# Kernel tuning notes

Measured on AMD Instinct MI355X. Metric: run time of the kernel, lower is better.

The kernel has to match this reference:

```python
import jax, jax.numpy as jnp
import numpy as np

B, S, D, H = 4, 2048, 1024, 16
HD = D // H  # head dim = 64


def setup_inputs() -> dict:
    key = jax.random.key(0)
    ks = jax.random.split(key, 10)
    sd = 1.0 / np.sqrt(D)
    return {
        "x": jax.random.normal(ks[0], (B, S, D), jnp.float32),
        "Wq": jax.random.normal(ks[1], (D, D), jnp.float32) * sd,
        "Wk": jax.random.normal(ks[2], (D, D), jnp.float32) * sd,
        "Wv": jax.random.normal(ks[3], (D, D), jnp.float32) * sd,
        "in_w": jax.random.normal(ks[4], (3 * D, D), jnp.float32) * sd,
        "in_b": jax.random.normal(ks[5], (3 * D,), jnp.float32) * 0.01,
        "out_w": jax.random.normal(ks[6], (D, D), jnp.float32) * sd,
        "out_b": jax.random.normal(ks[7], (D,), jnp.float32) * 0.01,
        "proj_w": jax.random.normal(ks[8], (D, D), jnp.float32) * sd,
        "proj_b": jax.random.normal(ks[9], (D,), jnp.float32) * 0.01,
    }


def _attn_block(x, Wq, Wk, Wv, in_w, in_b, out_w, out_b, proj_w, proj_b):
    b, s, d = x.shape
    # redundant pre-projections (bias-free)
    q = jnp.einsum('bsd,ed->bse', x, Wq)
    k = jnp.einsum('bsd,ed->bse', x, Wk)
    v = jnp.einsum('bsd,ed->bse', x, Wv)
    # MultiheadAttention internal in-projection (with bias)
    wq, wk, wv = in_w[:d], in_w[d:2 * d], in_w[2 * d:]
    bq, bk, bv = in_b[:d], in_b[d:2 * d], in_b[2 * d:]
    Q = jnp.einsum('bse,fe->bsf', q, wq) + bq
    K = jnp.einsum('bse,fe->bsf', k, wk) + bk
    V = jnp.einsum('bse,fe->bsf', v, wv) + bv
    # split heads -> [b, h, s, hd]
    Q = Q.reshape(b, s, H, HD).transpose(0, 2, 1, 3)
    K = K.reshape(b, s, H, HD).transpose(0, 2, 1, 3)
    V = V.reshape(b, s, H, HD).transpose(0, 2, 1, 3)
    scale = 1.0 / np.sqrt(HD)
    scores = jnp.einsum('bhqd,bhkd->bhqk', Q * scale, K)
    # FAITHFUL quirk: float tril mask (ones / zeros) is ADDED to scores,
    # exactly as torch does with a float attn_mask (not a -inf causal mask).
    mask = jnp.tril(jnp.ones((s, s), scores.dtype))
    scores = scores + mask
    A = jax.nn.softmax(scores, axis=-1)
    ctx = jnp.einsum('bhqk,bhkd->bhqd', A, V)
    ctx = ctx.transpose(0, 2, 1, 3).reshape(b, s, d)
    attn = jnp.einsum('bse,fe->bsf', ctx, out_w) + out_b  # out_proj
    out = jnp.einsum('bse,fe->bsf', attn, proj_w) + proj_b  # self.project
    return x + out


def reference(x, Wq, Wk, Wv, in_w, in_b, out_w, out_b, proj_w, proj_b):
    return _attn_block(x, Wq, Wk, Wv, in_w, in_b, out_w, out_b, proj_w, proj_b)
```

## Files before the change

kernel.cpp:

```cpp
#include <hip/hip_runtime.h>
#include <stdint.h>

typedef unsigned short u16;
typedef __attribute__((ext_vector_type(8))) short bfx8;
typedef __attribute__((ext_vector_type(4))) float fx4;
typedef __attribute__((ext_vector_type(16))) float fx16;

static __device__ __forceinline__ u16 f2b(float f) {
  union { float f; uint32_t u; } v; v.f = f;
  uint32_t r = v.u + 0x7fffu + ((v.u >> 16) & 1u);
  return (u16)(r >> 16);
}

static __device__ __forceinline__ uint32_t cvtpk(float lo, float hi) {
  uint32_t r;
  asm("v_cvt_pk_bf16_f32 %0, %1, %2" : "=v"(r) : "v"(lo), "v"(hi));
  return r;
}

static __device__ __forceinline__ float ex2(float x) {
  float r;
  asm("v_exp_f32 %0, %1" : "=v"(r) : "v"(x));
  return r;
}

static __device__ __forceinline__ void gload16(const void* g, void* lds) {
  __builtin_amdgcn_global_load_lds((const __attribute__((address_space(1))) uint32_t*)g,
                                   (__attribute__((address_space(3))) uint32_t*)lds,
                                   16, 0, 0);
}

__global__ __launch_bounds__(256) void f32_to_bf16_k(const float* __restrict__ in,
                                                     u16* __restrict__ out, int n) {
  int i = (blockIdx.x * 256 + threadIdx.x) * 8;
  if (i >= n) return;
  float4 a = *(const float4*)(in + i);
  float4 b = *(const float4*)(in + i + 4);
  bfx8 o;
  o[0]=(short)f2b(a.x); o[1]=(short)f2b(a.y); o[2]=(short)f2b(a.z); o[3]=(short)f2b(a.w);
  o[4]=(short)f2b(b.x); o[5]=(short)f2b(b.y); o[6]=(short)f2b(b.z); o[7]=(short)f2b(b.w);
  *(bfx8*)(out + i) = o;
}

struct TransArgs { const float* in[4]; u16* out[4]; };
__global__ __launch_bounds__(256) void transpose4_k(TransArgs ta) {
  const float* in = ta.in[blockIdx.z];
  u16* out = ta.out[blockIdx.z];
  __shared__ u16 t[64][65];
  const int bx = blockIdx.x * 64, by = blockIdx.y * 64;
  const int tid = threadIdx.x;
#pragma unroll
  for (int i = 0; i < 16; ++i) {
    int idx = tid + i * 256; int r = idx >> 6, c = idx & 63;
    t[c][r] = f2b(in[(size_t)(by + r) * 1024 + bx + c]);
  }
  __syncthreads();
#pragma unroll
  for (int i = 0; i < 16; ++i) {
    int idx = tid + i * 256; int r = idx >> 6, c = idx & 63;
    out[(size_t)(bx + r) * 1024 + by + c] = t[r][c];
  }
}

__global__ __launch_bounds__(256) void make_b2_k(const float* __restrict__ pw,
                                                 const float* __restrict__ ob,
                                                 const float* __restrict__ pb,
                                                 float* __restrict__ b2) {
  const int f = blockIdx.x, tid = threadIdx.x;
  float s = 0.f;
  for (int e = tid; e < 1024; e += 256) s += pw[(size_t)f * 1024 + e] * ob[e];
#pragma unroll
  for (int d = 1; d < 64; d <<= 1) s += __shfl_xor(s, d);
  __shared__ float red[4];
  if ((tid & 63) == 0) red[tid >> 6] = s;
  __syncthreads();
  if (tid == 0) b2[f] = red[0] + red[1] + red[2] + red[3] + pb[f];
}

static __device__ __forceinline__ void gemm_core(const u16* __restrict__ A,
                                                 const u16* __restrict__ Bt,
                                                 int K, int bm, int bn,
                                                 u16* As, u16* Bs, fx4 (&acc)[4][4]) {
  const int tid = threadIdx.x, w = tid >> 6, l = tid & 63, lm = l & 15, lk = l >> 4;
  const int wm = w >> 1, wn = w & 1;
  const int nkt = K >> 6;
  for (int kt = 0; kt < nkt; ++kt) {
#pragma unroll
    for (int i = 0; i < 4; ++i) {
      int off = i * 4096 + w * 1024;
      int loff = off + l * 16;
      int row = loff >> 7, cb = loff & 127;
      gload16((const char*)A + ((size_t)(bm * 128 + row) * K + kt * 64) * 2 + cb,
              (char*)As + off);
      gload16((const char*)Bt + ((size_t)(bn * 128 + row) * K + kt * 64) * 2 + cb,
              (char*)Bs + off);
    }
    __syncthreads();
#pragma unroll
    for (int kk = 0; kk < 2; ++kk) {
      bfx8 a[4], b[4];
#pragma unroll
      for (int mi = 0; mi < 4; ++mi)
        a[mi] = *(const bfx8*)((const char*)As + (wm * 64 + mi * 16 + lm) * 128 + lk * 16 + kk * 64);
#pragma unroll
      for (int nj = 0; nj < 4; ++nj)
        b[nj] = *(const bfx8*)((const char*)Bs + (wn * 64 + nj * 16 + lm) * 128 + lk * 16 + kk * 64);
#pragma unroll
      for (int mi = 0; mi < 4; ++mi)
#pragma unroll
        for (int nj = 0; nj < 4; ++nj)
          acc[mi][nj] = __builtin_amdgcn_mfma_f32_16x16x32_bf16(a[mi], b[nj], acc[mi][nj], 0, 0, 0);
    }
    __syncthreads();
  }
}

struct CombArgs { const u16* A[4]; const u16* Bt[4]; u16* C[4]; };
__global__ __launch_bounds__(256) void gemm_combine_k(CombArgs ca) {
  const int z = blockIdx.z;
  __shared__ u16 As[8192], Bs[8192];
  fx4 acc[4][4];
#pragma unroll
  for (int mi = 0; mi < 4; ++mi)
#pragma unroll
    for (int nj = 0; nj < 4; ++nj) acc[mi][nj] = 0.f;
  gemm_core(ca.A[z], ca.Bt[z], 1024, blockIdx.x, blockIdx.y, As, Bs, acc);
  const int tid = threadIdx.x, w = tid >> 6, l = tid & 63, lm = l & 15, lk = l >> 4;
  const int wm = w >> 1, wn = w & 1;
  u16* C = ca.C[z];
#pragma unroll
  for (int mi = 0; mi < 4; ++mi)
#pragma unroll
    for (int nj = 0; nj < 4; ++nj)
#pragma unroll
      for (int r = 0; r < 4; ++r) {
        int m = blockIdx.x * 128 + wm * 64 + mi * 16 + lk * 4 + r;
        int n = blockIdx.y * 128 + wn * 64 + nj * 16 + lm;
        C[(size_t)m * 1024 + n] = f2b(acc[mi][nj][r]);
      }
}

__global__ __launch_bounds__(256) void gemm_qkv_k(const u16* __restrict__ xb,
                                                  const u16* __restrict__ Wc,
                                                  const float* __restrict__ bias,
                                                  u16* __restrict__ Qh, u16* __restrict__ Kh,
                                                  u16* __restrict__ Vh) {
  const int bl = blockIdx.x;
  const int xcd = bl & 7, local = bl >> 3;
  const int bm = xcd * 8 + (local & 7);
  const int bn = local >> 3;
  __shared__ u16 As[8192], Bs[8192];
  fx4 acc[4][4];
#pragma unroll
  for (int mi = 0; mi < 4; ++mi)
#pragma unroll
    for (int nj = 0; nj < 4; ++nj) acc[mi][nj] = 0.f;
  gemm_core(xb, Wc, 1024, bm, bn, As, Bs, acc);
  const int tid = threadIdx.x, w = tid >> 6, l = tid & 63, lm = l & 15, lk = l >> 4;
  const int wm = w >> 1, wn = w & 1;
  const int t = bn >> 3;
  u16* dst = (t == 0) ? Qh : ((t == 1) ? Kh : Vh);
#pragma unroll
  for (int mi = 0; mi < 4; ++mi)
#pragma unroll
    for (int nj = 0; nj < 4; ++nj)
#pragma unroll
      for (int r = 0; r < 4; ++r) {
        int m = bm * 128 + wm * 64 + mi * 16 + lk * 4 + r;
        int n = bn * 128 + wn * 64 + nj * 16 + lm;
        float v = acc[mi][nj][r] + bias[n];
        int f = n & 1023, h = f >> 6, hd = f & 63, b = m >> 11, s = m & 2047;
        size_t hb = ((size_t)(b * 16 + h)) * 131072;
        size_t idx;
        if (t == 2) {
          int sl = s & 63, st = s >> 6;
          idx = hb + (size_t)st * 4096 + (size_t)(hd * 64 + (sl ^ ((hd & 7) << 3)));
        } else if (t == 1) {
          idx = hb + (size_t)s * 64 + (hd ^ ((s & 7) << 3));
        } else {
          idx = hb + (size_t)s * 64 + hd;
        }
        dst[idx] = f2b(v);
      }
}

__global__ __launch_bounds__(256) void gemm_final_k(const u16* __restrict__ ctx,
                                                    const u16* __restrict__ W2,
                                                    const float* __restrict__ b2,
                                                    const float* __restrict__ x,
                                                    float* __restrict__ out) {
  const int bl = blockIdx.x;
  const int xcd = bl & 7, local = bl >> 3;
  const int bm = xcd * 8 + (local & 7);
  const int bn = local >> 3;
  __shared__ u16 As[8192], Bs[8192];
  fx4 acc[4][4];
#pragma unroll
  for (int mi = 0; mi < 4; ++mi)
#pragma unroll
    for (int nj = 0; nj < 4; ++nj) acc[mi][nj] = 0.f;
  gemm_core(ctx, W2, 1024, bm, bn, As, Bs, acc);
  const int tid = threadIdx.x, w = tid >> 6, l = tid & 63, lm = l & 15, lk = l >> 4;
  const int wm = w >> 1, wn = w & 1;
#pragma unroll
  for (int mi = 0; mi < 4; ++mi)
#pragma unroll
    for (int nj = 0; nj < 4; ++nj)
#pragma unroll
      for (int r = 0; r < 4; ++r) {
        int m = bm * 128 + wm * 64 + mi * 16 + lk * 4 + r;
        int n = bn * 128 + wn * 64 + nj * 16 + lm;
        size_t idx = (size_t)m * 1024 + n;
        out[idx] = acc[mi][nj][r] + b2[n] + x[idx];
      }
}

__global__ __launch_bounds__(512, 4) void attn_k(const u16* __restrict__ Qh,
                                                 const u16* __restrict__ Kh,
                                                 const u16* __restrict__ Vh,
                                                 u16* __restrict__ ctx) {
  const int bl = blockIdx.x;
  const int wk = (bl & 7) * 64 + (bl >> 3);
  const int bh = wk >> 3, qt = wk & 7;
  const int tid = threadIdx.x, w = tid >> 6, l = tid & 63;
  const int ql = l & 31, h = l >> 5;
  __shared__ __align__(16) u16 Ks[2][4096];
  __shared__ __align__(16) u16 Vs[2][4096];

  const float SC = 0.18033688011112042f;
  const float MA = 1.4426950408889634f;
  const float THR = 11.541560327111708f;

  const size_t base = (size_t)bh * 131072;
  const int qb = qt * 256 + w * 32;
  const int q = qb + ql;
  bfx8 qf[4];
  {
    const u16* qp = Qh + base + (size_t)q * 64 + 8 * h;
    qf[0] = *(const bfx8*)(qp);
    qf[1] = *(const bfx8*)(qp + 16);
    qf[2] = *(const bfx8*)(qp + 32);
    qf[3] = *(const bfx8*)(qp + 48);
  }
  float m_run = -1024.f, l_part = 0.f;
  fx16 accO[2];
  accO[0] = 0.f; accO[1] = 0.f;

  const char* Kg = (const char*)(Kh + base);
  const char* Vg = (const char*)(Vh + base);
  const int o = tid * 16;
  const int sw8 = (ql & 7) << 4;

#define STAGE(t, s)                                            \
  {                                                            \
    gload16(Kg + (size_t)(t) * 8192 + o, (char*)Ks[s] + o);    \
    gload16(Vg + (size_t)(t) * 8192 + o, (char*)Vs[s] + o);    \
  }

  STAGE(0, 0);
  asm volatile("s_waitcnt vmcnt(0)" ::: "memory");
  __builtin_amdgcn_s_barrier();
  __builtin_amdgcn_sched_barrier(0);

  int cur = 0;
  for (int kt = 0; kt < 32; ++kt) {
    if (kt + 1 < 32) STAGE(kt + 1, cur ^ 1);
    __builtin_amdgcn_sched_barrier(0);

    const char* Kc = (const char*)Ks[cur];
    const char* Vc = (const char*)Vs[cur];

    fx16 sS[2];
    sS[0] = 0.f; sS[1] = 0.f;
    __builtin_amdgcn_s_setprio(1);
#pragma unroll
    for (int ks = 0; ks < 4; ++ks) {
      bfx8 kf0 = *(const bfx8*)(Kc + (0 * 32 + ql) * 128 + (((ks << 5) | (h << 4)) ^ sw8));
      bfx8 kf1 = *(const bfx8*)(Kc + (1 * 32 + ql) * 128 + (((ks << 5) | (h << 4)) ^ sw8));
      sS[0] = __builtin_amdgcn_mfma_f32_32x32x16_bf16(kf0, qf[ks], sS[0], 0, 0, 0);
      sS[1] = __builtin_amdgcn_mfma_f32_32x32x16_bf16(kf1, qf[ks], sS[1], 0, 0, 0);
    }
    __builtin_amdgcn_s_setprio(0);

    const int dk = kt - (qb >> 6);
    {
      float cO = -m_run, cI = cO + MA;
      if (dk < 0) {
#pragma unroll
        for (int r = 0; r < 16; ++r) {
          sS[0][r] = fmaf(sS[0][r], SC, cI);
          sS[1][r] = fmaf(sS[1][r], SC, cI);
        }
      } else if (dk > 0) {
#pragma unroll
        for (int r = 0; r < 16; ++r) {
          sS[0][r] = fmaf(sS[0][r], SC, cO);
          sS[1][r] = fmaf(sS[1][r], SC, cO);
        }
      } else {
#pragma unroll
        for (int kb = 0; kb < 2; ++kb)
#pragma unroll
          for (int r = 0; r < 16; ++r) {
            int key = kt * 64 + kb * 32 + (r & 3) + 8 * (r >> 2) + 4 * h;
            sS[kb][r] = fmaf(sS[kb][r], SC, (key <= q) ? cI : cO);
          }
      }
    }
    float mx;
    {
      float m0 = fmaxf(fmaxf(sS[0][0], sS[0][1]), fmaxf(sS[0][2], sS[0][3]));
      float m1 = fmaxf(fmaxf(sS[0][4], sS[0][5]), fmaxf(sS[0][6], sS[0][7]));
      float m2 = fmaxf(fmaxf(sS[0][8], sS[0][9]), fmaxf(sS[0][10], sS[0][11]));
      float m3 = fmaxf(fmaxf(sS[0][12], sS[0][13]), fmaxf(sS[0][14], sS[0][15]));
      float m4 = fmaxf(fmaxf(sS[1][0], sS[1][1]), fmaxf(sS[1][2], sS[1][3]));
      float m5 = fmaxf(fmaxf(sS[1][4], sS[1][5]), fmaxf(sS[1][6], sS[1][7]));
      float m6 = fmaxf(fmaxf(sS[1][8], sS[1][9]), fmaxf(sS[1][10], sS[1][11]));
      float m7 = fmaxf(fmaxf(sS[1][12], sS[1][13]), fmaxf(sS[1][14], sS[1][15]));
      mx = fmaxf(fmaxf(fmaxf(m0, m1), fmaxf(m2, m3)), fmaxf(fmaxf(m4, m5), fmaxf(m6, m7)));
    }
    float full = fmaxf(mx, __shfl_xor(mx, 32));
    if (!__all(full <= THR)) {
      float d = fmaxf(full, 0.f);
      float corr = ex2(-d);
      m_run += d;
      l_part *= corr;
#pragma unroll
      for (int r = 0; r < 16; ++r) {
        int rq = (r & 3) + 8 * (r >> 2) + 4 * h;
        float cr = __shfl(corr, (l & 32) | rq);
        accO[0][r] *= cr;
        accO[1][r] *= cr;
        sS[0][r] -= d;
        sS[1][r] -= d;
      }
    }
    fx16 tt;
#pragma unroll
    for (int r = 0; r < 16; ++r) {
      sS[0][r] = ex2(sS[0][r]);
      sS[1][r] = ex2(sS[1][r]);
      tt[r] = sS[0][r] + sS[1][r];
    }
    {
      float ls0 = tt[0] + tt[8],  ls1 = tt[1] + tt[9];
      float ls2 = tt[2] + tt[10], ls3 = tt[3] + tt[11];
      float ls4 = tt[4] + tt[12], ls5 = tt[5] + tt[13];
      float ls6 = tt[6] + tt[14], ls7 = tt[7] + tt[15];
      l_part += ((ls0 + ls4) + (ls1 + ls5)) + ((ls2 + ls6) + (ls3 + ls7));
    }
    uint32_t pw[8][2];
#pragma unroll
    for (int kb = 0; kb < 2; ++kb)
#pragma unroll
      for (int gg = 0; gg < 4; ++gg) {
        pw[kb * 4 + gg][0] = cvtpk(sS[kb][4 * gg + 0], sS[kb][4 * gg + 1]);
        pw[kb * 4 + gg][1] = cvtpk(sS[kb][4 * gg + 2], sS[kb][4 * gg + 3]);
      }

    __builtin_amdgcn_s_setprio(1);
#pragma unroll
    for (int ks = 0; ks < 4; ++ks) {
      union { uint32_t u[4]; bfx8 v; } pa;
#pragma unroll
      for (int p = 0; p < 2; ++p) {
        uint32_t contrib = h ? pw[2 * ks][p] : pw[2 * ks + 1][p];
        uint32_t rcv = __shfl_xor(contrib, 32);
        pa.u[p]     = h ? rcv : pw[2 * ks][p];
        pa.u[2 + p] = h ? pw[2 * ks + 1][p] : rcv;
      }
      bfx8 vf0 = *(const bfx8*)(Vc + (0 * 32 + ql) * 128 + (((ks << 5) | (h << 4)) ^ sw8));
      bfx8 vf1 = *(const bfx8*)(Vc + (1 * 32 + ql) * 128 + (((ks << 5) | (h << 4)) ^ sw8));
      accO[0] = __builtin_amdgcn_mfma_f32_32x32x16_bf16(pa.v, vf0, accO[0], 0, 0, 0);
      accO[1] = __builtin_amdgcn_mfma_f32_32x32x16_bf16(pa.v, vf1, accO[1], 0, 0, 0);
    }
    __builtin_amdgcn_s_setprio(0);

    asm volatile("s_waitcnt vmcnt(0)" ::: "memory");
    __builtin_amdgcn_s_barrier();
    __builtin_amdgcn_sched_barrier(0);
    cur ^= 1;
  }
#undef STAGE

  float inv = 1.0f / (l_part + __shfl_xor(l_part, 32));
  const int b = bh >> 4, hcol = bh & 15;
#pragma unroll
  for (int r = 0; r < 16; ++r) {
    int rq = (r & 3) + 8 * (r >> 2) + 4 * h;
    float invq = __shfl(inv, (l & 32) | rq);
    size_t rowb = ((size_t)b * 2048 + (qb + rq)) * 1024 + hcol * 64 + ql;
    ctx[rowb]      = f2b(accO[0][r] * invq);
    ctx[rowb + 32] = f2b(accO[1][r] * invq);
  }
}

extern "C" void kernel_launch(void* const* d_in, const int* in_sizes, int n_in,
                              void* d_out, int out_size, void* d_ws, size_t ws_size,
                              hipStream_t stream) {
  (void)in_sizes; (void)n_in; (void)out_size; (void)ws_size;
  const float* x      = (const float*)d_in[0];
  const float* Wq     = (const float*)d_in[1];
  const float* Wk     = (const float*)d_in[2];
  const float* Wv     = (const float*)d_in[3];
  const float* in_w   = (const float*)d_in[4];
  const float* in_b   = (const float*)d_in[5];
  const float* out_w  = (const float*)d_in[6];
  const float* out_b  = (const float*)d_in[7];
  const float* proj_w = (const float*)d_in[8];
  const float* proj_b = (const float*)d_in[9];
  float* out = (float*)d_out;

  char* ws = (char*)d_ws;
  const size_t MB = 1ull << 20;
  u16* xb   = (u16*)(ws);
  u16* ctx  = xb;
  u16* Qh   = (u16*)(ws + 16 * MB);
  u16* Kh   = (u16*)(ws + 32 * MB);
  u16* Vh   = (u16*)(ws + 48 * MB);
  u16* inwb = Kh;
  u16* tmpT = Vh;
  u16* pwb  = (u16*)(ws + 48 * MB + 8 * MB);
  u16* Wc   = (u16*)(ws + 64 * MB);
  u16* W2   = (u16*)(ws + 70 * MB);
  float* b2 = (float*)(ws + 72 * MB);

  f32_to_bf16_k<<<4096, 256, 0, stream>>>(x, xb, 8388608);
  f32_to_bf16_k<<<1536, 256, 0, stream>>>(in_w, inwb, 3145728);
  f32_to_bf16_k<<<512, 256, 0, stream>>>(proj_w, pwb, 1048576);

  TransArgs ta;
  ta.in[0] = Wq; ta.in[1] = Wk; ta.in[2] = Wv; ta.in[3] = out_w;
  for (int z = 0; z < 4; ++z) ta.out[z] = tmpT + (size_t)z * 1048576;
  transpose4_k<<<dim3(16, 16, 4), 256, 0, stream>>>(ta);

  CombArgs ca;
  ca.A[0] = inwb; ca.A[1] = inwb + 1048576; ca.A[2] = inwb + 2097152; ca.A[3] = pwb;
  for (int z = 0; z < 4; ++z) ca.Bt[z] = tmpT + (size_t)z * 1048576;
  ca.C[0] = Wc; ca.C[1] = Wc + 1048576; ca.C[2] = Wc + 2097152; ca.C[3] = W2;
  gemm_combine_k<<<dim3(8, 8, 4), 256, 0, stream>>>(ca);

  make_b2_k<<<1024, 256, 0, stream>>>(proj_w, out_b, proj_b, b2);

  gemm_qkv_k<<<1536, 256, 0, stream>>>(xb, Wc, in_b, Qh, Kh, Vh);
  attn_k<<<512, 512, 0, stream>>>(Qh, Kh, Vh, ctx);
  gemm_final_k<<<512, 256, 0, stream>>>(ctx, W2, b2, x, out);
}
```

Before: 266.2 us.

## Double attention K/V stage size, merge convert launches, bf16 residual read

The attention kernel now stages 128 keys per double-buffered step instead of 64 and processes them as two 64-key sub-tiles. This halves the number of wait-plus-barrier points per block, at the cost of doubling LDS per block, which may lower occupancy. The three fp32-to-bf16 conversion launches are merged into one kernel to cut launch overhead. When the workspace is large enough, ctx gets its own buffer and the final GEMM reads the residual from the bf16 copy of x instead of fp32 x. That halves residual traffic but adds bf16 rounding error to the output.

```diff
diff --git a/kernel.cpp b/kernel.cpp
--- a/kernel.cpp
+++ b/kernel.cpp
@@ -12,6 +12,11 @@
   return (u16)(r >> 16);
 }
 
+static __device__ __forceinline__ float b2f(u16 u) {
+  union { uint32_t u; float f; } v; v.u = ((uint32_t)u) << 16;
+  return v.f;
+}
+
 static __device__ __forceinline__ uint32_t cvtpk(float lo, float hi) {
   uint32_t r;
   asm("v_cvt_pk_bf16_f32 %0, %1, %2" : "=v"(r) : "v"(lo), "v"(hi));
@@ -30,16 +35,21 @@
                                    16, 0, 0);
 }
 
-__global__ __launch_bounds__(256) void f32_to_bf16_k(const float* __restrict__ in,
-                                                     u16* __restrict__ out, int n) {
-  int i = (blockIdx.x * 256 + threadIdx.x) * 8;
-  if (i >= n) return;
-  float4 a = *(const float4*)(in + i);
-  float4 b = *(const float4*)(in + i + 4);
+struct Cv3 { const float* in0; u16* out0; const float* in1; u16* out1;
+             const float* in2; u16* out2; };
+__global__ __launch_bounds__(256) void convert3_k(Cv3 a) {
+  const int b = blockIdx.x;
+  const float* in; u16* out; int i;
+  if (b < 4096)      { in = a.in0; out = a.out0; i = b; }
+  else if (b < 5632) { in = a.in1; out = a.out1; i = b - 4096; }
+  else               { in = a.in2; out = a.out2; i = b - 5632; }
+  int idx = (i * 256 + threadIdx.x) * 8;
+  float4 x = *(const float4*)(in + idx);
+  float4 y = *(const float4*)(in + idx + 4);
   bfx8 o;
-  o[0]=(short)f2b(a.x); o[1]=(short)f2b(a.y); o[2]=(short)f2b(a.z); o[3]=(short)f2b(a.w);
-  o[4]=(short)f2b(b.x); o[5]=(short)f2b(b.y); o[6]=(short)f2b(b.z); o[7]=(short)f2b(b.w);
-  *(bfx8*)(out + i) = o;
+  o[0]=(short)f2b(x.x); o[1]=(short)f2b(x.y); o[2]=(short)f2b(x.z); o[3]=(short)f2b(x.w);
+  o[4]=(short)f2b(y.x); o[5]=(short)f2b(y.y); o[6]=(short)f2b(y.z); o[7]=(short)f2b(y.w);
+  *(bfx8*)(out + idx) = o;
 }
 
 struct TransArgs { const float* in[4]; u16* out[4]; };
@@ -188,6 +198,7 @@
                                                     const u16* __restrict__ W2,
                                                     const float* __restrict__ b2,
                                                     const float* __restrict__ x,
+                                                    const u16* __restrict__ resid16,
                                                     float* __restrict__ out) {
   const int bl = blockIdx.x;
   const int xcd = bl & 7, local = bl >> 3;
@@ -211,7 +222,8 @@
         int m = bm * 128 + wm * 64 + mi * 16 + lk * 4 + r;
         int n = bn * 128 + wn * 64 + nj * 16 + lm;
         size_t idx = (size_t)m * 1024 + n;
-        out[idx] = acc[mi][nj][r] + b2[n] + x[idx];
+        float res = resid16 ? b2f(resid16[idx]) : x[idx];
+        out[idx] = acc[mi][nj][r] + b2[n] + res;
       }
 }
 
@@ -224,8 +236,8 @@
   const int bh = wk >> 3, qt = wk & 7;
   const int tid = threadIdx.x, w = tid >> 6, l = tid & 63;
   const int ql = l & 31, h = l >> 5;
-  __shared__ __align__(16) u16 Ks[2][4096];
-  __shared__ __align__(16) u16 Vs[2][4096];
+  __shared__ __align__(16) u16 Ks[2][8192];
+  __shared__ __align__(16) u16 Vs[2][8192];
 
   const float SC = 0.18033688011112042f;
   const float MA = 1.4426950408889634f;
@@ -251,10 +263,12 @@
   const int o = tid * 16;
   const int sw8 = (ql & 7) << 4;
 
-#define STAGE(t, s)                                            \
-  {                                                            \
-    gload16(Kg + (size_t)(t) * 8192 + o, (char*)Ks[s] + o);    \
-    gload16(Vg + (size_t)(t) * 8192 + o, (char*)Vs[s] + o);    \
+#define STAGE(t, s)                                                          \
+  {                                                                          \
+    gload16(Kg + (size_t)(t) * 16384 + o,        (char*)Ks[s] + o);          \
+    gload16(Kg + (size_t)(t) * 16384 + o + 8192, (char*)Ks[s] + o + 8192);   \
+    gload16(Vg + (size_t)(t) * 16384 + o,        (char*)Vs[s] + o);          \
+    gload16(Vg + (size_t)(t) * 16384 + o + 8192, (char*)Vs[s] + o + 8192);   \
   }
 
   STAGE(0, 0);
@@ -263,118 +277,122 @@
   __builtin_amdgcn_sched_barrier(0);
 
   int cur = 0;
-  for (int kt = 0; kt < 32; ++kt) {
-    if (kt + 1 < 32) STAGE(kt + 1, cur ^ 1);
+  for (int kt = 0; kt < 16; ++kt) {
+    if (kt + 1 < 16) STAGE(kt + 1, cur ^ 1);
     __builtin_amdgcn_sched_barrier(0);
 
-    const char* Kc = (const char*)Ks[cur];
-    const char* Vc = (const char*)Vs[cur];
-
-    fx16 sS[2];
-    sS[0] = 0.f; sS[1] = 0.f;
-    __builtin_amdgcn_s_setprio(1);
-#pragma unroll
-    for (int ks = 0; ks < 4; ++ks) {
-      bfx8 kf0 = *(const bfx8*)(Kc + (0 * 32 + ql) * 128 + (((ks << 5) | (h << 4)) ^ sw8));
-      bfx8 kf1 = *(const bfx8*)(Kc + (1 * 32 + ql) * 128 + (((ks << 5) | (h << 4)) ^ sw8));
-      sS[0] = __builtin_amdgcn_mfma_f32_32x32x16_bf16(kf0, qf[ks], sS[0], 0, 0, 0);
-      sS[1] = __builtin_amdgcn_mfma_f32_32x32x16_bf16(kf1, qf[ks], sS[1], 0, 0, 0);
+#pragma unroll
+    for (int sub = 0; sub < 2; ++sub) {
+      const char* Kc = (const char*)Ks[cur] + sub * 8192;
+      const char* Vc = (const char*)Vs[cur] + sub * 8192;
+      const int kt2 = kt * 2 + sub;
+
+      fx16 sS[2];
+      sS[0] = 0.f; sS[1] = 0.f;
+      __builtin_amdgcn_s_setprio(1);
+#pragma unroll
+      for (int ks = 0; ks < 4; ++ks) {
+        bfx8 kf0 = *(const bfx8*)(Kc + (0 * 32 + ql) * 128 + (((ks << 5) | (h << 4)) ^ sw8));
+        bfx8 kf1 = *(const bfx8*)(Kc + (1 * 32 + ql) * 128 + (((ks << 5) | (h << 4)) ^ sw8));
+        sS[0] = __builtin_amdgcn_mfma_f32_32x32x16_bf16(kf0, qf[ks], sS[0], 0, 0, 0);
+        sS[1] = __builtin_amdgcn_mfma_f32_32x32x16_bf16(kf1, qf[ks], sS[1], 0, 0, 0);
+      }
+      __builtin_amdgcn_s_setprio(0);
+
+      const int dk = kt2 - (qb >> 6);
+      {
+        float cO = -m_run, cI = cO + MA;
+        if (dk < 0) {
+#pragma unroll
+          for (int r = 0; r < 16; ++r) {
+            sS[0][r] = fmaf(sS[0][r], SC, cI);
+            sS[1][r] = fmaf(sS[1][r], SC, cI);
+          }
+        } else if (dk > 0) {
+#pragma unroll
+          for (int r = 0; r < 16; ++r) {
+            sS[0][r] = fmaf(sS[0][r], SC, cO);
+            sS[1][r] = fmaf(sS[1][r], SC, cO);
+          }
+        } else {
+#pragma unroll
+          for (int kb = 0; kb < 2; ++kb)
+#pragma unroll
+            for (int r = 0; r < 16; ++r) {
+              int key = kt2 * 64 + kb * 32 + (r & 3) + 8 * (r >> 2) + 4 * h;
+              sS[kb][r] = fmaf(sS[kb][r], SC, (key <= q) ? cI : cO);
+            }
+        }
+      }
+      float mx;
+      {
+        float m0 = fmaxf(fmaxf(sS[0][0], sS[0][1]), fmaxf(sS[0][2], sS[0][3]));
+        float m1 = fmaxf(fmaxf(sS[0][4], sS[0][5]), fmaxf(sS[0][6], sS[0][7]));
+        float m2 = fmaxf(fmaxf(sS[0][8], sS[0][9]), fmaxf(sS[0][10], sS[0][11]));
+        float m3 = fmaxf(fmaxf(sS[0][12], sS[0][13]), fmaxf(sS[0][14], sS[0][15]));
+        float m4 = fmaxf(fmaxf(sS[1][0], sS[1][1]), fmaxf(sS[1][2], sS[1][3]));
+        float m5 = fmaxf(fmaxf(sS[1][4], sS[1][5]), fmaxf(sS[1][6], sS[1][7]));
+        float m6 = fmaxf(fmaxf(sS[1][8], sS[1][9]), fmaxf(sS[1][10], sS[1][11]));
+        float m7 = fmaxf(fmaxf(sS[1][12], sS[1][13]), fmaxf(sS[1][14], sS[1][15]));
+        mx = fmaxf(fmaxf(fmaxf(m0, m1), fmaxf(m2, m3)), fmaxf(fmaxf(m4, m5), fmaxf(m6, m7)));
+      }
+      float full = fmaxf(mx, __shfl_xor(mx, 32));
+      if (!__all(full <= THR)) {
+        float d = fmaxf(full, 0.f);
+        float corr = ex2(-d);
+        m_run += d;
+        l_part *= corr;
+#pragma unroll
+        for (int r = 0; r < 16; ++r) {
+          int rq = (r & 3) + 8 * (r >> 2) + 4 * h;
+          float cr = __shfl(corr, (l & 32) | rq);
+          accO[0][r] *= cr;
+          accO[1][r] *= cr;
+          sS[0][r] -= d;
+          sS[1][r] -= d;
+        }
+      }
+      fx16 tt;
+#pragma unroll
+      for (int r = 0; r < 16; ++r) {
+        sS[0][r] = ex2(sS[0][r]);
+        sS[1][r] = ex2(sS[1][r]);
+        tt[r] = sS[0][r] + sS[1][r];
+      }
+      {
+        float ls0 = tt[0] + tt[8],  ls1 = tt[1] + tt[9];
+        float ls2 = tt[2] + tt[10], ls3 = tt[3] + tt[11];
+        float ls4 = tt[4] + tt[12], ls5 = tt[5] + tt[13];
+        float ls6 = tt[6] + tt[14], ls7 = tt[7] + tt[15];
+        l_part += ((ls0 + ls4) + (ls1 + ls5)) + ((ls2 + ls6) + (ls3 + ls7));
+      }
+      uint32_t pw[8][2];
+#pragma unroll
+      for (int kb = 0; kb < 2; ++kb)
+#pragma unroll
+        for (int gg = 0; gg < 4; ++gg) {
+          pw[kb * 4 + gg][0] = cvtpk(sS[kb][4 * gg + 0], sS[kb][4 * gg + 1]);
+          pw[kb * 4 + gg][1] = cvtpk(sS[kb][4 * gg + 2], sS[kb][4 * gg + 3]);
+        }
+
+      __builtin_amdgcn_s_setprio(1);
+#pragma unroll
+      for (int ks = 0; ks < 4; ++ks) {
+        union { uint32_t u[4]; bfx8 v; } pa;
+#pragma unroll
+        for (int p = 0; p < 2; ++p) {
+          uint32_t contrib = h ? pw[2 * ks][p] : pw[2 * ks + 1][p];
+          uint32_t rcv = __shfl_xor(contrib, 32);
+          pa.u[p]     = h ? rcv : pw[2 * ks][p];
+          pa.u[2 + p] = h ? pw[2 * ks + 1][p] : rcv;
+        }
+        bfx8 vf0 = *(const bfx8*)(Vc + (0 * 32 + ql) * 128 + (((ks << 5) | (h << 4)) ^ sw8));
+        bfx8 vf1 = *(const bfx8*)(Vc + (1 * 32 + ql) * 128 + (((ks << 5) | (h << 4)) ^ sw8));
+        accO[0] = __builtin_amdgcn_mfma_f32_32x32x16_bf16(pa.v, vf0, accO[0], 0, 0, 0);
+        accO[1] = __builtin_amdgcn_mfma_f32_32x32x16_bf16(pa.v, vf1, accO[1], 0, 0, 0);
+      }
+      __builtin_amdgcn_s_setprio(0);
     }
-    __builtin_amdgcn_s_setprio(0);
-
-    const int dk = kt - (qb >> 6);
-    {
-      float cO = -m_run, cI = cO + MA;
-      if (dk < 0) {
-#pragma unroll
-        for (int r = 0; r < 16; ++r) {
-          sS[0][r] = fmaf(sS[0][r], SC, cI);
-          sS[1][r] = fmaf(sS[1][r], SC, cI);
-        }
-      } else if (dk > 0) {
-#pragma unroll
-        for (int r = 0; r < 16; ++r) {
-          sS[0][r] = fmaf(sS[0][r], SC, cO);
-          sS[1][r] = fmaf(sS[1][r], SC, cO);
-        }
-      } else {
-#pragma unroll
-        for (int kb = 0; kb < 2; ++kb)
-#pragma unroll
-          for (int r = 0; r < 16; ++r) {
-            int key = kt * 64 + kb * 32 + (r & 3) + 8 * (r >> 2) + 4 * h;
-            sS[kb][r] = fmaf(sS[kb][r], SC, (key <= q) ? cI : cO);
-          }
-      }
-    }
-    float mx;
-    {
-      float m0 = fmaxf(fmaxf(sS[0][0], sS[0][1]), fmaxf(sS[0][2], sS[0][3]));
-      float m1 = fmaxf(fmaxf(sS[0][4], sS[0][5]), fmaxf(sS[0][6], sS[0][7]));
-      float m2 = fmaxf(fmaxf(sS[0][8], sS[0][9]), fmaxf(sS[0][10], sS[0][11]));
-      float m3 = fmaxf(fmaxf(sS[0][12], sS[0][13]), fmaxf(sS[0][14], sS[0][15]));
-      float m4 = fmaxf(fmaxf(sS[1][0], sS[1][1]), fmaxf(sS[1][2], sS[1][3]));
-      float m5 = fmaxf(fmaxf(sS[1][4], sS[1][5]), fmaxf(sS[1][6], sS[1][7]));
-      float m6 = fmaxf(fmaxf(sS[1][8], sS[1][9]), fmaxf(sS[1][10], sS[1][11]));
-      float m7 = fmaxf(fmaxf(sS[1][12], sS[1][13]), fmaxf(sS[1][14], sS[1][15]));
-      mx = fmaxf(fmaxf(fmaxf(m0, m1), fmaxf(m2, m3)), fmaxf(fmaxf(m4, m5), fmaxf(m6, m7)));
-    }
-    float full = fmaxf(mx, __shfl_xor(mx, 32));
-    if (!__all(full <= THR)) {
-      float d = fmaxf(full, 0.f);
-      float corr = ex2(-d);
-      m_run += d;
-      l_part *= corr;
-#pragma unroll
-      for (int r = 0; r < 16; ++r) {
-        int rq = (r & 3) + 8 * (r >> 2) + 4 * h;
-        float cr = __shfl(corr, (l & 32) | rq);
-        accO[0][r] *= cr;
-        accO[1][r] *= cr;
-        sS[0][r] -= d;
-        sS[1][r] -= d;
-      }
-    }
-    fx16 tt;
-#pragma unroll
-    for (int r = 0; r < 16; ++r) {
-      sS[0][r] = ex2(sS[0][r]);
-      sS[1][r] = ex2(sS[1][r]);
-      tt[r] = sS[0][r] + sS[1][r];
-    }
-    {
-      float ls0 = tt[0] + tt[8],  ls1 = tt[1] + tt[9];
-      float ls2 = tt[2] + tt[10], ls3 = tt[3] + tt[11];
-      float ls4 = tt[4] + tt[12], ls5 = tt[5] + tt[13];
-      float ls6 = tt[6] + tt[14], ls7 = tt[7] + tt[15];
-      l_part += ((ls0 + ls4) + (ls1 + ls5)) + ((ls2 + ls6) + (ls3 + ls7));
-    }
-    uint32_t pw[8][2];
-#pragma unroll
-    for (int kb = 0; kb < 2; ++kb)
-#pragma unroll
-      for (int gg = 0; gg < 4; ++gg) {
-        pw[kb * 4 + gg][0] = cvtpk(sS[kb][4 * gg + 0], sS[kb][4 * gg + 1]);
-        pw[kb * 4 + gg][1] = cvtpk(sS[kb][4 * gg + 2], sS[kb][4 * gg + 3]);
-      }
-
-    __builtin_amdgcn_s_setprio(1);
-#pragma unroll
-    for (int ks = 0; ks < 4; ++ks) {
-      union { uint32_t u[4]; bfx8 v; } pa;
-#pragma unroll
-      for (int p = 0; p < 2; ++p) {
-        uint32_t contrib = h ? pw[2 * ks][p] : pw[2 * ks + 1][p];
-        uint32_t rcv = __shfl_xor(contrib, 32);
-        pa.u[p]     = h ? rcv : pw[2 * ks][p];
-        pa.u[2 + p] = h ? pw[2 * ks + 1][p] : rcv;
-      }
-      bfx8 vf0 = *(const bfx8*)(Vc + (0 * 32 + ql) * 128 + (((ks << 5) | (h << 4)) ^ sw8));
-      bfx8 vf1 = *(const bfx8*)(Vc + (1 * 32 + ql) * 128 + (((ks << 5) | (h << 4)) ^ sw8));
-      accO[0] = __builtin_amdgcn_mfma_f32_32x32x16_bf16(pa.v, vf0, accO[0], 0, 0, 0);
-      accO[1] = __builtin_amdgcn_mfma_f32_32x32x16_bf16(pa.v, vf1, accO[1], 0, 0, 0);
-    }
-    __builtin_amdgcn_s_setprio(0);
 
     asm volatile("s_waitcnt vmcnt(0)" ::: "memory");
     __builtin_amdgcn_s_barrier();
@@ -398,7 +416,7 @@
 extern "C" void kernel_launch(void* const* d_in, const int* in_sizes, int n_in,
                               void* d_out, int out_size, void* d_ws, size_t ws_size,
                               hipStream_t stream) {
-  (void)in_sizes; (void)n_in; (void)out_size; (void)ws_size;
+  (void)in_sizes; (void)n_in; (void)out_size;
   const float* x      = (const float*)d_in[0];
   const float* Wq     = (const float*)d_in[1];
   const float* Wk     = (const float*)d_in[2];
@@ -414,7 +432,6 @@
   char* ws = (char*)d_ws;
   const size_t MB = 1ull << 20;
   u16* xb   = (u16*)(ws);
-  u16* ctx  = xb;
   u16* Qh   = (u16*)(ws + 16 * MB);
   u16* Kh   = (u16*)(ws + 32 * MB);
   u16* Vh   = (u16*)(ws + 48 * MB);
@@ -424,10 +441,13 @@
   u16* Wc   = (u16*)(ws + 64 * MB);
   u16* W2   = (u16*)(ws + 70 * MB);
   float* b2 = (float*)(ws + 72 * MB);
-
-  f32_to_bf16_k<<<4096, 256, 0, stream>>>(x, xb, 8388608);
-  f32_to_bf16_k<<<1536, 256, 0, stream>>>(in_w, inwb, 3145728);
-  f32_to_bf16_k<<<512, 256, 0, stream>>>(proj_w, pwb, 1048576);
+  const bool bigws = ws_size >= 90 * MB;
+  u16* ctx = bigws ? (u16*)(ws + 73 * MB) : xb;
+  const u16* resid16 = bigws ? xb : nullptr;
+
+  Cv3 cv; cv.in0 = x; cv.out0 = xb; cv.in1 = in_w; cv.out1 = inwb;
+  cv.in2 = proj_w; cv.out2 = pwb;
+  convert3_k<<<6144, 256, 0, stream>>>(cv);
 
   TransArgs ta;
   ta.in[0] = Wq; ta.in[1] = Wk; ta.in[2] = Wv; ta.in[3] = out_w;
@@ -444,5 +464,5 @@
 
   gemm_qkv_k<<<1536, 256, 0, stream>>>(xb, Wc, in_b, Qh, Kh, Vh);
   attn_k<<<512, 512, 0, stream>>>(Qh, Kh, Vh, ctx);
-  gemm_final_k<<<512, 256, 0, stream>>>(ctx, W2, b2, x, out);
-}
+  gemm_final_k<<<512, 256, 0, stream>>>(ctx, W2, b2, x, resid16, out);
+}
```

Measured after the change: 367.7 us. +38.1%, slower.
